# Kernel optimization log

Measured on AMD Instinct MI355X. Metric: run time of the kernel, lower is better.

The kernel has to match this reference:

```python
import jax, jax.numpy as jnp
import numpy as np

B, T, D = 4, 4096, 1024
H = 16
DH = D // H
F = 4096
EPS = 1e-5


def _layernorm(x, gamma, beta):
    mu = jnp.mean(x, axis=-1, keepdims=True)
    var = jnp.var(x, axis=-1, keepdims=True)
    return (x - mu) * jax.lax.rsqrt(var + EPS) * gamma + beta


def setup_inputs() -> dict:
    key = jax.random.key(0)
    ks = jax.random.split(key, 10)
    s = 0.02
    return {
        "x": jax.random.normal(ks[0], (B, T, D), dtype=jnp.float32),
        "Wqkv": jax.random.normal(ks[1], (D, 3 * D), dtype=jnp.float32) * s,
        "bqkv": jnp.zeros((3 * D,), dtype=jnp.float32),
        "Wo": jax.random.normal(ks[2], (D, D), dtype=jnp.float32) * s,
        "bo": jnp.zeros((D,), dtype=jnp.float32),
        "W1": jax.random.normal(ks[3], (D, F), dtype=jnp.float32) * s,
        "b1": jnp.zeros((F,), dtype=jnp.float32),
        "W2": jax.random.normal(ks[4], (F, D), dtype=jnp.float32) * s,
        "b2": jnp.zeros((D,), dtype=jnp.float32),
        "g1": jnp.ones((D,), dtype=jnp.float32),
        "be1": jnp.zeros((D,), dtype=jnp.float32),
        "g2": jnp.ones((D,), dtype=jnp.float32),
        "be2": jnp.zeros((D,), dtype=jnp.float32),
    }


def reference(x, Wqkv, bqkv, Wo, bo, W1, b1, W2, b2, g1, be1, g2, be2):
    # fused QKV projection: [B,T,3D]
    qkv = jnp.einsum("btd,de->bte", x, Wqkv) + bqkv
    q, k, v = jnp.split(qkv, 3, axis=-1)
    # [B,H,T,DH]
    q = q.reshape(B, T, H, DH).transpose(0, 2, 1, 3)
    k = k.reshape(B, T, H, DH).transpose(0, 2, 1, 3)
    v = v.reshape(B, T, H, DH).transpose(0, 2, 1, 3)
    scores = jnp.einsum("bhqd,bhkd->bhqk", q, k) / jnp.sqrt(jnp.float32(DH))
    attn = jax.nn.softmax(scores, axis=-1)
    ctx = jnp.einsum("bhqk,bhkd->bhqd", attn, v)
    ctx = ctx.transpose(0, 2, 1, 3).reshape(B, T, D)
    # output projection + residual + post-LN
    x = _layernorm(x + (jnp.einsum("btd,de->bte", ctx, Wo) + bo), g1, be1)
    # FFN (exact GELU, torch default) + residual + post-LN
    h = jax.nn.gelu(jnp.einsum("btd,df->btf", x, W1) + b1, approximate=False)
    ffn = jnp.einsum("btf,fd->btd", h, W2) + b2
    return _layernorm(x + ffn, g2, be2)
```

## Files before the change

kernel.cpp:

```cpp
#include <hip/hip_runtime.h>
#include <math.h>

typedef unsigned short u16;
typedef unsigned int   u32;
typedef __attribute__((ext_vector_type(8))) short short8;
typedef __attribute__((ext_vector_type(4))) float f32x4;

#define B_  4
#define T_  4096
#define D_  1024
#define H_  16
#define DH_ 64
#define F_  4096
#define EPS_ 1e-5f
#define QKV_LD (3 * D_)

#define QSCALE_ 0.18033688011112042f

__device__ __forceinline__ float b2f(u16 v) {
    union { u32 u; float f; } x; x.u = ((u32)v) << 16; return x.f;
}
__device__ __forceinline__ u16 f2b(float f) {
    union { u32 u; float f; } x; x.f = f;
    u32 r = (x.u >> 16) & 1u;
    return (u16)((x.u + 0x7fffu + r) >> 16);
}

__device__ __forceinline__ float ex2(float x) {
    float r;
    asm("v_exp_f32 %0, %1" : "=v"(r) : "v"(x));
    return r;
}
__device__ __forceinline__ float rcp_(float x) {
    float r;
    asm("v_rcp_f32 %0, %1" : "=v"(r) : "v"(x));
    return r;
}
__device__ __forceinline__ u32 cvtpk(float lo, float hi) {
    u32 r;
    asm("v_cvt_pk_bf16_f32 %0, %1, %2" : "=v"(r) : "v"(lo), "v"(hi));
    return r;
}
template<int CTRL>
__device__ __forceinline__ u32 dppu(u32 v) {
    return (u32)__builtin_amdgcn_update_dpp(0, (int)v, CTRL, 0xF, 0xF, true);
}

__device__ __forceinline__ float gelu_erf(float x) {
    const float z = fabsf(x) * 0.70710678118654752f;
    const float t = rcp_(1.0f + 0.3275911f * z);
    float poly = 1.061405429f;
    poly = poly * t - 1.453152027f;
    poly = poly * t + 1.421413741f;
    poly = poly * t - 0.284496736f;
    poly = poly * t + 0.254829592f;
    poly = poly * t;
    const float e = ex2(-z * z * 1.4426950408889634f);
    const float erfz = 1.0f - poly * e;
    const float se = copysignf(erfz, x);
    return 0.5f * x * (1.0f + se);
}

__device__ __forceinline__ void gll16(const u16* g, u16* ldsbase) {
    __builtin_amdgcn_global_load_lds(
        (const __attribute__((address_space(1))) void*)g,
        (__attribute__((address_space(3))) void*)ldsbase, 16, 0, 0);
}

__global__ __launch_bounds__(256) void conv_bf16_kernel(
    const float* __restrict__ in, u16* __restrict__ out)
{
    const int i = blockIdx.x * 256 + threadIdx.x;
    float4 v = ((const float4*)in)[i];
    ushort4 o;
    o.x = f2b(v.x); o.y = f2b(v.y); o.z = f2b(v.z); o.w = f2b(v.w);
    ((ushort4*)out)[i] = o;
}

__global__ __launch_bounds__(256) void transpose_bf16_kernel(
    const float* __restrict__ W, u16* __restrict__ Wt, int R, int C)
{
    __shared__ float tile[32][33];
    const int bx = blockIdx.x * 32;
    const int by = blockIdx.y * 32;
    const int tx = threadIdx.x & 31, ty = threadIdx.x >> 5;
#pragma unroll
    for (int p = 0; p < 4; ++p)
        tile[ty + p * 8][tx] = W[(size_t)(by + ty + p * 8) * C + bx + tx];
    __syncthreads();
#pragma unroll
    for (int p = 0; p < 4; ++p)
        Wt[(size_t)(bx + ty + p * 8) * R + by + tx] = f2b(tile[tx][ty + p * 8]);
}

template<bool CBF, int KU>
__global__ __launch_bounds__(256) void mfma_gemm(
    const u16* __restrict__ A, int lda,
    const u16* __restrict__ Bt, int ldbt,
    const float* __restrict__ bias,
    void* __restrict__ Cv, int ldc,
    int K, int act, int acc, int qcols)
{
    __shared__ __align__(16) u16 Al[KU][128 * 32];
    __shared__ __align__(16) u16 Bl[KU][128 * 32];

    const int tid  = threadIdx.x;
    const int lane = tid & 63, wave = tid >> 6;
    const int quad = lane >> 4, l16 = lane & 15;

    const int gx = gridDim.x;
    const int nwg = gx * gridDim.y;
    const int lin = blockIdx.y * gx + blockIdx.x;
    const int wg  = (lin & 7) * (nwg >> 3) + (lin >> 3);
    const int m0 = (wg / gx) * 128, n0 = (wg % gx) * 128;

    const int wm = (wave >> 1) * 64, wn = (wave & 1) * 64;

    int srow[2], sgk[2];
#pragma unroll
    for (int t = 0; t < 2; ++t) {
        const int c = wave * 128 + t * 64 + lane;
        srow[t] = c >> 2;
        sgk[t] = ((c & 3) ^ ((srow[t] >> 1) & 3)) * 8;
    }
    const u16* Ag = A  + (size_t)m0 * lda;
    const u16* Bg = Bt + (size_t)n0 * ldbt;
    const int apos = (quad ^ ((l16 >> 1) & 3)) * 8;

    f32x4 accr[4][4];
#pragma unroll
    for (int i = 0; i < 4; ++i)
#pragma unroll
        for (int j = 0; j < 4; ++j)
            accr[i][j] = (f32x4)(0.0f);

    for (int k0 = 0; k0 < K; k0 += 32 * KU) {
        __syncthreads();
#pragma unroll
        for (int h = 0; h < KU; ++h)
#pragma unroll
            for (int t = 0; t < 2; ++t) {
                gll16(Ag + (size_t)srow[t] * lda  + k0 + h * 32 + sgk[t],
                      &Al[h][(wave * 128 + t * 64) * 8]);
                gll16(Bg + (size_t)srow[t] * ldbt + k0 + h * 32 + sgk[t],
                      &Bl[h][(wave * 128 + t * 64) * 8]);
            }
        __syncthreads();

#pragma unroll
        for (int h = 0; h < KU; ++h) {
            short8 af[4], bf[4];
#pragma unroll
            for (int i = 0; i < 4; ++i)
                af[i] = *(const short8*)&Al[h][(wm + i * 16 + l16) * 32 + apos];
#pragma unroll
            for (int j = 0; j < 4; ++j)
                bf[j] = *(const short8*)&Bl[h][(wn + j * 16 + l16) * 32 + apos];
#pragma unroll
            for (int i = 0; i < 4; ++i)
#pragma unroll
                for (int j = 0; j < 4; ++j)
                    accr[i][j] = __builtin_amdgcn_mfma_f32_16x16x32_bf16(
                        af[i], bf[j], accr[i][j], 0, 0, 0);
        }
    }

#pragma unroll
    for (int j = 0; j < 4; ++j) {
        const int cc = n0 + wn + j * 16 + l16;
        float bv = acc ? 0.0f : bias[cc];
        const float sc = (cc < qcols) ? QSCALE_ : 1.0f;
#pragma unroll
        for (int i = 0; i < 4; ++i) {
#pragma unroll
            for (int r = 0; r < 4; ++r) {
                const int rr = m0 + wm + i * 16 + quad * 4 + r;
                float v = (accr[i][j][r] + bv) * sc;
                if (act == 1)
                    v = gelu_erf(v);
                if (CBF) {
                    ((u16*)Cv)[(size_t)rr * ldc + cc] = f2b(v);
                } else {
                    float* dst = (float*)Cv + (size_t)rr * ldc + cc;
                    if (acc) v += *dst;
                    *dst = v;
                }
            }
        }
    }
}

__global__ __launch_bounds__(256) void attn_mfma_kernel(
    const u16* __restrict__ qkv, u16* __restrict__ ctx)
{
    __shared__ u16 Ks[64 * 72];
    __shared__ u16 Vt[64 * 72];

    const int tid  = threadIdx.x;
    const int lane = tid & 63, wave = tid >> 6;
    const int quad = lane >> 4, l16 = lane & 15;
    const bool hi  = lane >= 32;
    const int bpa  = (lane ^ 32) << 2;

    const int gx = gridDim.x, gy = gridDim.y;
    const int nwg = gx * gy * gridDim.z;
    const int lin = (blockIdx.z * gy + blockIdx.y) * gx + blockIdx.x;
    const int wg  = (lin & 7) * (nwg >> 3) + (lin >> 3);
    const int q0 = (wg % gx) * 128;
    const int h  = (wg / gx) % gy;
    const int b  = wg / (gx * gy);

    short8 ones8;
#pragma unroll
    for (int i = 0; i < 8; ++i) ones8[i] = (short)0x3F80;

    short8 aq[2][2];
    {
        const u16* qb = qkv + (size_t)(b * T_ + q0 + wave * 32) * QKV_LD + h * DH_;
#pragma unroll
        for (int u = 0; u < 2; ++u)
#pragma unroll
            for (int s = 0; s < 2; ++s)
                aq[u][s] = *(const short8*)(qb + (size_t)(u * 16 + l16) * QKV_LD + s * 32 + quad * 8);
    }

    const int srow = tid >> 3;
    const int scol = (tid & 7) * 8;
    const int odd8 = srow & 1;
    const u16* kg = qkv + (size_t)(b * T_) * QKV_LD + D_     + h * DH_;
    const u16* vg = qkv + (size_t)(b * T_) * QKV_LD + 2 * D_ + h * DH_;

    short8 kreg[2], vreg[2];
#pragma unroll
    for (int half = 0; half < 2; ++half) {
        const int row = srow + half * 32;
        kreg[half] = *(const short8*)(kg + (size_t)row * QKV_LD + scol);
        vreg[half] = *(const short8*)(vg + (size_t)row * QKV_LD + scol);
    }

    f32x4 o_acc[2][4];
#pragma unroll
    for (int u = 0; u < 2; ++u)
#pragma unroll
        for (int nt = 0; nt < 4; ++nt)
            o_acc[u][nt] = (f32x4)(0.0f);
    f32x4 l_acc[2];
    l_acc[0] = (f32x4)(0.0f);
    l_acc[1] = (f32x4)(0.0f);

    for (int kt = 0; kt < T_; kt += 64) {
        __syncthreads();
#pragma unroll
        for (int half = 0; half < 2; ++half) {
            const int row = srow + half * 32;
            *(short8*)&Ks[row * 72 + scol] = kreg[half];

            union { short8 s; u32 w[4]; } vv;
            vv.s = vreg[half];
            const u32 ws0 = dppu<0x118>(vv.w[0]);
            const u32 ws1 = dppu<0x118>(vv.w[1]);
            const u32 sl2 = dppu<0x108>(vv.w[2]);
            const u32 sl3 = dppu<0x108>(vv.w[3]);
            const int rowb = row & ~1;
            const int sw = ((rowb & ~12) | ((rowb & 4) << 1) | ((rowb & 8) >> 1))
                           ^ ((rowb & 16) >> 2);
            const int koff = sw ^ scol;
#pragma unroll
            for (int J = 0; J < 4; ++J) {
                const u32 wj   = vv.w[J >> 1];
                const u32 wj4  = vv.w[2 + (J >> 1)];
                const u32 wsj  = (J >> 1) ? ws1 : ws0;
                const u32 slj4 = (J >> 1) ? sl3 : sl2;
                const u32 selfJ  = (J & 1) ? (wj   >> 16) : (wj   & 0xFFFFu);
                const u32 selfJ4 = (J & 1) ? (wj4  >> 16) : (wj4  & 0xFFFFu);
                const u32 nbrJ   = (J & 1) ? (wsj  >> 16) : (wsj  & 0xFFFFu);
                const u32 nbrJ4  = (J & 1) ? (slj4 >> 16) : (slj4 & 0xFFFFu);
                const u32 lo16 = odd8 ? nbrJ4  : selfJ;
                const u32 hi16 = odd8 ? selfJ4 : nbrJ;
                const int dh = scol + J + (odd8 ? 4 : 0);
                *(u32*)&Vt[dh * 72 + koff] = lo16 | (hi16 << 16);
            }
        }
        __syncthreads();

        if (kt + 64 < T_) {
#pragma unroll
            for (int half = 0; half < 2; ++half) {
                const int row = srow + half * 32;
                kreg[half] = *(const short8*)(kg + (size_t)(kt + 64 + row) * QKV_LD + scol);
                vreg[half] = *(const short8*)(vg + (size_t)(kt + 64 + row) * QKV_LD + scol);
            }
        }

        f32x4 sa[2][4];
#pragma unroll
        for (int u = 0; u < 2; ++u)
#pragma unroll
            for (int nt = 0; nt < 4; ++nt)
                sa[u][nt] = (f32x4)(0.0f);
        __builtin_amdgcn_s_setprio(1);
#pragma unroll
        for (int s = 0; s < 2; ++s) {
            short8 kb[4];
#pragma unroll
            for (int nt = 0; nt < 4; ++nt)
                kb[nt] = *(const short8*)&Ks[(nt * 16 + l16) * 72 + s * 32 + quad * 8];
#pragma unroll
            for (int u = 0; u < 2; ++u)
#pragma unroll
                for (int nt = 0; nt < 4; ++nt)
                    sa[u][nt] = __builtin_amdgcn_mfma_f32_16x16x32_bf16(
                        kb[nt], aq[u][s], sa[u][nt], 0, 0, 0);
        }
        __builtin_amdgcn_s_setprio(0);

        u32 pk[2][4][2];
#pragma unroll
        for (int u = 0; u < 2; ++u)
#pragma unroll
            for (int nt = 0; nt < 4; ++nt)
#pragma unroll
                for (int w = 0; w < 2; ++w)
                    pk[u][nt][w] = cvtpk(ex2(sa[u][nt][2 * w]),
                                         ex2(sa[u][nt][2 * w + 1]));

        __builtin_amdgcn_s_setprio(1);
#pragma unroll
        for (int s = 0; s < 2; ++s) {
            short8 vb[4];
#pragma unroll
            for (int nt = 0; nt < 4; ++nt) {
                const int dh = nt * 16 + l16;
                vb[nt] = *(const short8*)&Vt[dh * 72 + ((s * 32 + quad * 8) ^ (dh & 56))];
            }
#pragma unroll
            for (int u = 0; u < 2; ++u) {
                union { u32 w[4]; short8 v; } pb;
                pb.w[0] = hi ? pk[u][2 * s + 1][0] : pk[u][2 * s][0];
                pb.w[1] = hi ? pk[u][2 * s + 1][1] : pk[u][2 * s][1];
                const u32 c0 = hi ? pk[u][2 * s][0] : pk[u][2 * s + 1][0];
                const u32 c1 = hi ? pk[u][2 * s][1] : pk[u][2 * s + 1][1];
                pb.w[2] = (u32)__builtin_amdgcn_ds_bpermute(bpa, (int)c0);
                pb.w[3] = (u32)__builtin_amdgcn_ds_bpermute(bpa, (int)c1);
                l_acc[u] = __builtin_amdgcn_mfma_f32_16x16x32_bf16(
                    ones8, pb.v, l_acc[u], 0, 0, 0);
#pragma unroll
                for (int nt = 0; nt < 4; ++nt)
                    o_acc[u][nt] = __builtin_amdgcn_mfma_f32_16x16x32_bf16(
                        vb[nt], pb.v, o_acc[u][nt], 0, 0, 0);
            }
        }
        __builtin_amdgcn_s_setprio(0);
    }

#pragma unroll
    for (int u = 0; u < 2; ++u) {
        const float inv = rcp_(l_acc[u][0]);
        const size_t qrow = (size_t)(b * T_ + q0 + wave * 32 + u * 16 + l16);
#pragma unroll
        for (int nt = 0; nt < 4; ++nt) {
            uint2 o;
            o.x = cvtpk(o_acc[u][nt][0] * inv, o_acc[u][nt][1] * inv);
            o.y = cvtpk(o_acc[u][nt][2] * inv, o_acc[u][nt][3] * inv);
            *(uint2*)&ctx[qrow * D_ + h * DH_ + nt * 16 + quad * 4] = o;
        }
    }
}

template<bool ABF, bool BBF, bool OBF>
__global__ __launch_bounds__(256) void add_ln_kernel(
    const void* __restrict__ av, const void* __restrict__ bv,
    const float* __restrict__ g, const float* __restrict__ be,
    void* __restrict__ outv)
{
    const int row = blockIdx.x;
    const int tid = threadIdx.x;

    float v[4];
    if (ABF) {
        ushort4 va = *(const ushort4*)((const u16*)av + (size_t)row * D_ + tid * 4);
        v[0] = b2f(va.x); v[1] = b2f(va.y); v[2] = b2f(va.z); v[3] = b2f(va.w);
    } else {
        float4 va = *(const float4*)((const float*)av + (size_t)row * D_ + tid * 4);
        v[0] = va.x; v[1] = va.y; v[2] = va.z; v[3] = va.w;
    }
    if (BBF) {
        ushort4 vb = *(const ushort4*)((const u16*)bv + (size_t)row * D_ + tid * 4);
        v[0] += b2f(vb.x); v[1] += b2f(vb.y); v[2] += b2f(vb.z); v[3] += b2f(vb.w);
    } else {
        float4 vb = *(const float4*)((const float*)bv + (size_t)row * D_ + tid * 4);
        v[0] += vb.x; v[1] += vb.y; v[2] += vb.z; v[3] += vb.w;
    }

    float s  = v[0] + v[1] + v[2] + v[3];
    float ss = v[0]*v[0] + v[1]*v[1] + v[2]*v[2] + v[3]*v[3];
#pragma unroll
    for (int off = 32; off > 0; off >>= 1) {
        s  += __shfl_down(s,  off, 64);
        ss += __shfl_down(ss, off, 64);
    }
    __shared__ float ws[4], wss[4], stats[2];
    const int wave = tid >> 6, lane = tid & 63;
    if (lane == 0) { ws[wave] = s; wss[wave] = ss; }
    __syncthreads();
    if (tid == 0) {
        float ts  = ws[0] + ws[1] + ws[2] + ws[3];
        float tss = wss[0] + wss[1] + wss[2] + wss[3];
        float mu  = ts * (1.0f / D_);
        float var = tss * (1.0f / D_) - mu * mu;
        stats[0] = mu;
        stats[1] = rsqrtf(var + EPS_);
    }
    __syncthreads();
    const float mu = stats[0], rs = stats[1];

    const float4 g4  = *(const float4*)(g  + tid * 4);
    const float4 be4 = *(const float4*)(be + tid * 4);
    float gg[4]  = {g4.x, g4.y, g4.z, g4.w};
    float beb[4] = {be4.x, be4.y, be4.z, be4.w};
    if (OBF) {
        ushort4 o;
        o.x = f2b((v[0] - mu) * rs * gg[0] + beb[0]);
        o.y = f2b((v[1] - mu) * rs * gg[1] + beb[1]);
        o.z = f2b((v[2] - mu) * rs * gg[2] + beb[2]);
        o.w = f2b((v[3] - mu) * rs * gg[3] + beb[3]);
        *(ushort4*)((u16*)outv + (size_t)row * D_ + tid * 4) = o;
    } else {
        float4 o;
        o.x = (v[0] - mu) * rs * gg[0] + beb[0];
        o.y = (v[1] - mu) * rs * gg[1] + beb[1];
        o.z = (v[2] - mu) * rs * gg[2] + beb[2];
        o.w = (v[3] - mu) * rs * gg[3] + beb[3];
        *(float4*)((float*)outv + (size_t)row * D_ + tid * 4) = o;
    }
}

extern "C" void kernel_launch(void* const* d_in, const int* in_sizes, int n_in,
                              void* d_out, int out_size, void* d_ws, size_t ws_size,
                              hipStream_t stream)
{
    const float* x    = (const float*)d_in[0];
    const float* Wqkv = (const float*)d_in[1];
    const float* bqkv = (const float*)d_in[2];
    const float* Wo   = (const float*)d_in[3];
    const float* bo   = (const float*)d_in[4];
    const float* W1   = (const float*)d_in[5];
    const float* b1   = (const float*)d_in[6];
    const float* W2   = (const float*)d_in[7];
    const float* b2   = (const float*)d_in[8];
    const float* g1   = (const float*)d_in[9];
    const float* be1  = (const float*)d_in[10];
    const float* g2   = (const float*)d_in[11];
    const float* be2  = (const float*)d_in[12];
    float* out = (float*)d_out;

    const int M = B_ * T_;
    char* ws = (char*)d_ws;
    char* sc = (char*)d_out;

    u16*   qkvB   = (u16*)ws;
    u16*   ctxB   = (u16*)(ws + (size_t)100663296);
    float* proj   = (float*)ws;
    u16*   x1B    = (u16*)(ws + (size_t)100663296);
    u16*   hchunk = (u16*)ws;
    u16*   ffnB   = (u16*)(ws + (size_t)67108864);

    u16* xB    = (u16*)sc;
    u16* WqkvT = (u16*)(sc + (size_t)33554432);
    u16* WoT   = (u16*)(sc + (size_t)39845888);
    u16* W1T   = (u16*)(sc + (size_t)41943040);
    u16* W2T   = (u16*)(sc + (size_t)50331648);

    dim3 blk(256);

    conv_bf16_kernel<<<dim3(M * D_ / 1024), blk, 0, stream>>>(x, xB);
    transpose_bf16_kernel<<<dim3(3 * D_ / 32, D_ / 32), blk, 0, stream>>>(Wqkv, WqkvT, D_, 3 * D_);
    transpose_bf16_kernel<<<dim3(D_ / 32, D_ / 32), blk, 0, stream>>>(Wo, WoT, D_, D_);
    transpose_bf16_kernel<<<dim3(F_ / 32, D_ / 32), blk, 0, stream>>>(W1, W1T, D_, F_);
    transpose_bf16_kernel<<<dim3(D_ / 32, F_ / 32), blk, 0, stream>>>(W2, W2T, F_, D_);

    mfma_gemm<true, 1><<<dim3(3 * D_ / 128, M / 128), blk, 0, stream>>>(
        xB, D_, WqkvT, D_, bqkv, qkvB, 3 * D_, D_, 0, 0, D_);

    attn_mfma_kernel<<<dim3(T_ / 128, H_, B_), blk, 0, stream>>>(qkvB, ctxB);

    mfma_gemm<false, 1><<<dim3(D_ / 128, M / 128), blk, 0, stream>>>(
        ctxB, D_, WoT, D_, bo, proj, D_, D_, 0, 0, 0);

    add_ln_kernel<false, false, true><<<dim3(M), blk, 0, stream>>>(x, proj, g1, be1, x1B);

    for (int mc = 0; mc < 2; ++mc) {
        const size_t m0 = (size_t)mc * 8192;
        mfma_gemm<true, 1><<<dim3(F_ / 128, 8192 / 128), blk, 0, stream>>>(
            x1B + m0 * D_, D_, W1T, D_, b1, hchunk, F_, D_, 1, 0, 0);
        mfma_gemm<true, 2><<<dim3(D_ / 128, 8192 / 128), blk, 0, stream>>>(
            hchunk, F_, W2T, F_, b2, ffnB + m0 * D_, D_, F_, 0, 0, 0);
    }

    add_ln_kernel<true, true, false><<<dim3(M), blk, 0, stream>>>(x1B, ffnB, g2, be2, out);
}
```

Before: 1.025 ms.

## Double-buffer K/V LDS tiles in attention to drop one barrier per iteration

The attention kernel now keeps two LDS slots for K and transposed V. The next tile is written into the alternate slot after the current tile's MFMA work, so each iteration needs one barrier instead of two. This aims to cut synchronization stalls and let LDS writes overlap with other waves' compute. In exchange, LDS use per block doubles, which could lower occupancy.

After: 1.112 ms. +8.5%, slower.

```diff
diff --git a/kernel.cpp b/kernel.cpp
--- a/kernel.cpp
+++ b/kernel.cpp
@@ -193,8 +193,8 @@
 __global__ __launch_bounds__(256) void attn_mfma_kernel(
     const u16* __restrict__ qkv, u16* __restrict__ ctx)
 {
-    __shared__ u16 Ks[64 * 72];
-    __shared__ u16 Vt[64 * 72];
+    __shared__ u16 Ks[2][64 * 72];
+    __shared__ u16 Vt[2][64 * 72];
 
     const int tid  = threadIdx.x;
     const int lane = tid & 63, wave = tid >> 6;
@@ -230,6 +230,39 @@
     const u16* kg = qkv + (size_t)(b * T_) * QKV_LD + D_     + h * DH_;
     const u16* vg = qkv + (size_t)(b * T_) * QKV_LD + 2 * D_ + h * DH_;
 
+#define STAGE_TILE(slot) do {                                                  \
+        _Pragma("unroll")                                                      \
+        for (int half = 0; half < 2; ++half) {                                 \
+            const int row = srow + half * 32;                                  \
+            *(short8*)&Ks[slot][row * 72 + scol] = kreg[half];                 \
+            union { short8 s; u32 w[4]; } vv;                                  \
+            vv.s = vreg[half];                                                 \
+            const u32 ws0 = dppu<0x118>(vv.w[0]);                              \
+            const u32 ws1 = dppu<0x118>(vv.w[1]);                              \
+            const u32 sl2 = dppu<0x108>(vv.w[2]);                              \
+            const u32 sl3 = dppu<0x108>(vv.w[3]);                              \
+            const int rowb = row & ~1;                                         \
+            const int sw = ((rowb & ~12) | ((rowb & 4) << 1) | ((rowb & 8) >> 1)) \
+                           ^ ((rowb & 16) >> 2);                               \
+            const int koff = sw ^ scol;                                        \
+            _Pragma("unroll")                                                  \
+            for (int J = 0; J < 4; ++J) {                                      \
+                const u32 wj   = vv.w[J >> 1];                                 \
+                const u32 wj4  = vv.w[2 + (J >> 1)];                           \
+                const u32 wsj  = (J >> 1) ? ws1 : ws0;                         \
+                const u32 slj4 = (J >> 1) ? sl3 : sl2;                         \
+                const u32 selfJ  = (J & 1) ? (wj   >> 16) : (wj   & 0xFFFFu);  \
+                const u32 selfJ4 = (J & 1) ? (wj4  >> 16) : (wj4  & 0xFFFFu);  \
+                const u32 nbrJ   = (J & 1) ? (wsj  >> 16) : (wsj  & 0xFFFFu);  \
+                const u32 nbrJ4  = (J & 1) ? (slj4 >> 16) : (slj4 & 0xFFFFu);  \
+                const u32 lo16 = odd8 ? nbrJ4  : selfJ;                        \
+                const u32 hi16 = odd8 ? selfJ4 : nbrJ;                         \
+                const int dh = scol + J + (odd8 ? 4 : 0);                      \
+                *(u32*)&Vt[slot][dh * 72 + koff] = lo16 | (hi16 << 16);        \
+            }                                                                  \
+        }                                                                      \
+    } while (0)
+
     short8 kreg[2], vreg[2];
 #pragma unroll
     for (int half = 0; half < 2; ++half) {
@@ -237,6 +270,8 @@
         kreg[half] = *(const short8*)(kg + (size_t)row * QKV_LD + scol);
         vreg[half] = *(const short8*)(vg + (size_t)row * QKV_LD + scol);
     }
+    STAGE_TILE(0);
+    __syncthreads();
 
     f32x4 o_acc[2][4];
 #pragma unroll
@@ -249,41 +284,10 @@
     l_acc[1] = (f32x4)(0.0f);
 
     for (int kt = 0; kt < T_; kt += 64) {
-        __syncthreads();
-#pragma unroll
-        for (int half = 0; half < 2; ++half) {
-            const int row = srow + half * 32;
-            *(short8*)&Ks[row * 72 + scol] = kreg[half];
-
-            union { short8 s; u32 w[4]; } vv;
-            vv.s = vreg[half];
-            const u32 ws0 = dppu<0x118>(vv.w[0]);
-            const u32 ws1 = dppu<0x118>(vv.w[1]);
-            const u32 sl2 = dppu<0x108>(vv.w[2]);
-            const u32 sl3 = dppu<0x108>(vv.w[3]);
-            const int rowb = row & ~1;
-            const int sw = ((rowb & ~12) | ((rowb & 4) << 1) | ((rowb & 8) >> 1))
-                           ^ ((rowb & 16) >> 2);
-            const int koff = sw ^ scol;
-#pragma unroll
-            for (int J = 0; J < 4; ++J) {
-                const u32 wj   = vv.w[J >> 1];
-                const u32 wj4  = vv.w[2 + (J >> 1)];
-                const u32 wsj  = (J >> 1) ? ws1 : ws0;
-                const u32 slj4 = (J >> 1) ? sl3 : sl2;
-                const u32 selfJ  = (J & 1) ? (wj   >> 16) : (wj   & 0xFFFFu);
-                const u32 selfJ4 = (J & 1) ? (wj4  >> 16) : (wj4  & 0xFFFFu);
-                const u32 nbrJ   = (J & 1) ? (wsj  >> 16) : (wsj  & 0xFFFFu);
-                const u32 nbrJ4  = (J & 1) ? (slj4 >> 16) : (slj4 & 0xFFFFu);
-                const u32 lo16 = odd8 ? nbrJ4  : selfJ;
-                const u32 hi16 = odd8 ? selfJ4 : nbrJ;
-                const int dh = scol + J + (odd8 ? 4 : 0);
-                *(u32*)&Vt[dh * 72 + koff] = lo16 | (hi16 << 16);
-            }
-        }
-        __syncthreads();
-
-        if (kt + 64 < T_) {
+        const int cur = (kt >> 6) & 1;
+        const bool more = (kt + 64 < T_);
+
+        if (more) {
 #pragma unroll
             for (int half = 0; half < 2; ++half) {
                 const int row = srow + half * 32;
@@ -304,7 +308,7 @@
             short8 kb[4];
 #pragma unroll
             for (int nt = 0; nt < 4; ++nt)
-                kb[nt] = *(const short8*)&Ks[(nt * 16 + l16) * 72 + s * 32 + quad * 8];
+                kb[nt] = *(const short8*)&Ks[cur][(nt * 16 + l16) * 72 + s * 32 + quad * 8];
 #pragma unroll
             for (int u = 0; u < 2; ++u)
 #pragma unroll
@@ -331,7 +335,7 @@
 #pragma unroll
             for (int nt = 0; nt < 4; ++nt) {
                 const int dh = nt * 16 + l16;
-                vb[nt] = *(const short8*)&Vt[dh * 72 + ((s * 32 + quad * 8) ^ (dh & 56))];
+                vb[nt] = *(const short8*)&Vt[cur][dh * 72 + ((s * 32 + quad * 8) ^ (dh & 56))];
             }
 #pragma unroll
             for (int u = 0; u < 2; ++u) {
@@ -351,7 +355,13 @@
             }
         }
         __builtin_amdgcn_s_setprio(0);
-    }
+
+        if (more) {
+            STAGE_TILE(cur ^ 1);
+            __syncthreads();
+        }
+    }
+#undef STAGE_TILE
 
 #pragma unroll
     for (int u = 0; u < 2; ++u) {
```

## Double attention workgroup to 512 threads covering 256 query rows per block

Applied to the files above, without the earlier changes.

The attention kernel now launches 8 waves per workgroup, each still handling 32 query rows, so one block covers 256 queries instead of 128. Each thread stages one K/V row per tile instead of two, and every K/V tile loaded into shared memory is reused by twice as many waves. This halves the number of blocks and the total global K/V traffic, at the cost of fewer workgroups in the grid and heavier barrier synchronisation across 8 waves.

Result: no change. 1.014 ms (-1.1%).

```diff
diff --git a/kernel.cpp b/kernel.cpp
--- a/kernel.cpp
+++ b/kernel.cpp
@@ -190,7 +190,7 @@
     }
 }
 
-__global__ __launch_bounds__(256) void attn_mfma_kernel(
+__global__ __launch_bounds__(512) void attn_mfma_kernel(
     const u16* __restrict__ qkv, u16* __restrict__ ctx)
 {
     __shared__ u16 Ks[64 * 72];
@@ -206,7 +206,7 @@
     const int nwg = gx * gy * gridDim.z;
     const int lin = (blockIdx.z * gy + blockIdx.y) * gx + blockIdx.x;
     const int wg  = (lin & 7) * (nwg >> 3) + (lin >> 3);
-    const int q0 = (wg % gx) * 128;
+    const int q0 = (wg % gx) * 256;
     const int h  = (wg / gx) % gy;
     const int b  = wg / (gx * gy);
 
@@ -230,13 +230,9 @@
     const u16* kg = qkv + (size_t)(b * T_) * QKV_LD + D_     + h * DH_;
     const u16* vg = qkv + (size_t)(b * T_) * QKV_LD + 2 * D_ + h * DH_;
 
-    short8 kreg[2], vreg[2];
-#pragma unroll
-    for (int half = 0; half < 2; ++half) {
-        const int row = srow + half * 32;
-        kreg[half] = *(const short8*)(kg + (size_t)row * QKV_LD + scol);
-        vreg[half] = *(const short8*)(vg + (size_t)row * QKV_LD + scol);
-    }
+    short8 kreg, vreg;
+    kreg = *(const short8*)(kg + (size_t)srow * QKV_LD + scol);
+    vreg = *(const short8*)(vg + (size_t)srow * QKV_LD + scol);
 
     f32x4 o_acc[2][4];
 #pragma unroll
@@ -250,18 +246,16 @@
 
     for (int kt = 0; kt < T_; kt += 64) {
         __syncthreads();
-#pragma unroll
-        for (int half = 0; half < 2; ++half) {
-            const int row = srow + half * 32;
-            *(short8*)&Ks[row * 72 + scol] = kreg[half];
+        {
+            *(short8*)&Ks[srow * 72 + scol] = kreg;
 
             union { short8 s; u32 w[4]; } vv;
-            vv.s = vreg[half];
+            vv.s = vreg;
             const u32 ws0 = dppu<0x118>(vv.w[0]);
             const u32 ws1 = dppu<0x118>(vv.w[1]);
             const u32 sl2 = dppu<0x108>(vv.w[2]);
             const u32 sl3 = dppu<0x108>(vv.w[3]);
-            const int rowb = row & ~1;
+            const int rowb = srow & ~1;
             const int sw = ((rowb & ~12) | ((rowb & 4) << 1) | ((rowb & 8) >> 1))
                            ^ ((rowb & 16) >> 2);
             const int koff = sw ^ scol;
@@ -284,12 +278,8 @@
         __syncthreads();
 
         if (kt + 64 < T_) {
-#pragma unroll
-            for (int half = 0; half < 2; ++half) {
-                const int row = srow + half * 32;
-                kreg[half] = *(const short8*)(kg + (size_t)(kt + 64 + row) * QKV_LD + scol);
-                vreg[half] = *(const short8*)(vg + (size_t)(kt + 64 + row) * QKV_LD + scol);
-            }
+            kreg = *(const short8*)(kg + (size_t)(kt + 64 + srow) * QKV_LD + scol);
+            vreg = *(const short8*)(vg + (size_t)(kt + 64 + srow) * QKV_LD + scol);
         }
 
         f32x4 sa[2][4];
@@ -482,7 +472,7 @@
     mfma_gemm<true, 1><<<dim3(3 * D_ / 128, M / 128), blk, 0, stream>>>(
         xB, D_, WqkvT, D_, bqkv, qkvB, 3 * D_, D_, 0, 0, D_);
 
-    attn_mfma_kernel<<<dim3(T_ / 128, H_, B_), blk, 0, stream>>>(qkvB, ctxB);
+    attn_mfma_kernel<<<dim3(T_ / 256, H_, B_), dim3(512), 0, stream>>>(qkvB, ctxB);
 
     mfma_gemm<false, 1><<<dim3(D_ / 128, M / 128), blk, 0, stream>>>(
         ctxB, D_, WoT, D_, bo, proj, D_, D_, 0, 0, 0);
```
